# Kernel tuning notes

Hardware: AMD Instinct MI355X
Metric: run time of the kernel (lower is better)

The kernel has to match this reference:

```python
import jax, jax.numpy as jnp
import numpy as np

D = 4
R = 6
P = 2 * R + 1          # 13, fine match window
N = P * P              # 169
MR = 12
MP = 2 * MR + 1        # 25, coarse search window
DIL_INT = 15


def corr_sampler(t, r, Pp, dil):
    """SpatialCorrelationSampler(kernel_size=1, patch_size=Pp, dilation_patch=dil).
    t, r: (b,c,h,w). Returns (b,Pp,Pp,h,w): corr[b,p,q,y,x] = sum_c t[b,c,y,x]*r[b,c,y+dil*(p-R),x+dil*(q-R)] (zero pad)."""
    Rr = (Pp - 1) // 2
    pad = Rr * dil
    b, c, h, w = t.shape
    rp = jnp.pad(r, ((0, 0), (0, 0), (pad, pad), (pad, pad)))
    d = (jnp.arange(Pp) - Rr) * dil
    yi = jnp.arange(h)[None, :] + d[:, None] + pad      # (Pp,h)
    xi = jnp.arange(w)[None, :] + d[:, None] + pad      # (Pp,w)
    g = rp[:, :, yi[:, None, :, None], xi[None, :, None, :]]  # (b,c,Pp,Pp,h,w)
    return jnp.einsum('bchw,bcpqhw->bpqhw', t, g)


def bilinear_patch(src, py, px):
    """deform_im2col: bilinear-sample a PxP patch around (x+off_x+dx, y+off_y+dy).
    src (b,c,h,w); py (b,P,1,h,w); px (b,1,P,h,w) float coords. Returns (b,c,P,P,h,w)."""
    b, c, h, w = src.shape
    y0 = jnp.floor(py); x0 = jnp.floor(px)
    wy = py - y0; wx = px - x0
    y0 = y0.astype(jnp.int32); x0 = x0.astype(jnp.int32)

    def corner(yi, xi, wgt):
        valid = (yi >= 0) & (yi < h) & (xi >= 0) & (xi < w)
        yc = jnp.clip(yi, 0, h - 1)
        xc = jnp.clip(xi, 0, w - 1)
        v = jax.vmap(lambda im, a, bb: im[:, a, bb])(src, yc, xc)  # (b,c,P,P,h,w)
        return v * (wgt * valid)[:, None]

    out = corner(y0, x0, (1 - wy) * (1 - wx))
    out = out + corner(y0, x0 + 1, (1 - wy) * wx)
    out = out + corner(y0 + 1, x0, wy * (1 - wx))
    out = out + corner(y0 + 1, x0 + 1, wy * wx)
    return out


def unfold_patches(src, Pp):
    """F.unfold(src, kernel_size=Pp, padding=Rr) -> (b,c,Pp,Pp,h,w)."""
    Rr = (Pp - 1) // 2
    b, c, h, w = src.shape
    sp = jnp.pad(src, ((0, 0), (0, 0), (Rr, Rr), (Rr, Rr)))
    yi = jnp.arange(h)[None, :] + jnp.arange(Pp)[:, None]
    xi = jnp.arange(w)[None, :] + jnp.arange(Pp)[:, None]
    return sp[:, :, yi[:, None, :, None], xi[None, :, None, :]]


def _forward(feats_r, feats_t, quantized_r, nsearch, dirates):
    nref = feats_r.shape[0]
    b, c, h, w = feats_t.shape
    f32 = feats_t.dtype
    dy = (jnp.arange(P) - R).astype(f32)
    gy, gx = jnp.meshgrid(jnp.arange(-MR, MR + 1).astype(f32),
                          jnp.arange(-MR, MR + 1).astype(f32), indexing='ij')
    corrs = []
    py = px = None
    for si in range(nsearch):
        d = dirates[si]
        cc = corr_sampler(feats_t, feats_r[si], MP, d)                     # (b,MP,MP,h,w)
        cc = jax.nn.softmax(cc.reshape(b, MP * MP, h * w), axis=1).reshape(b, MP, MP, h, w)
        off_x = jnp.einsum('bpqhw,pq->bhw', cc, gx) * d                    # soft-argmax offsets
        off_y = jnp.einsum('bpqhw,pq->bhw', cc, gy) * d
        # sample coords: (b,P,1,h,w) / (b,1,P,h,w)
        py = (off_y + jnp.arange(h).astype(f32)[None, :, None])[:, None, None] + dy[:, None, None, None]
        px = (off_x + jnp.arange(w).astype(f32)[None, None, :])[:, None, None] + dy[None, :, None, None]
        col = bilinear_patch(feats_r[si], py, px)                          # (b,c,P,P,h,w)
        corrs.append(jnp.einsum('bchw,bcpqhw->bpqhw', feats_t, col).reshape(b, N, h * w))
    for ind in range(nsearch, nref):
        corrs.append(corr_sampler(feats_t, feats_r[ind], P, 1).reshape(b, N, h * w))
    corr = jax.nn.softmax(jnp.concatenate(corrs, 1), axis=1)               # (b,nref*N,hw)
    qr = quantized_r[:, :, :, ::D, ::D]                                    # prep(): (nref,b,C,h,w)
    cols = []
    for i in range(nsearch):
        # NOTE: faithful to original -- uses offset0 from the LAST coarse-search iteration
        cols.append(bilinear_patch(qr[i], py, px).reshape(b, -1, N, h * w))
    for i in range(nsearch, nref):
        cols.append(unfold_patches(qr[i], P).reshape(b, -1, N, h * w))
    image_uf = jnp.concatenate(cols, 2)                                    # (b,C,nref*N,hw)
    out = jnp.einsum('bnx,bcnx->bcx', corr, image_uf)
    return out.reshape(b, qr.shape[2], h, w)


def reference(feats_r, feats_t, quantized_r, ref_index, current_ind):
    gaps = [int(current_ind) - int(x) for x in np.asarray(ref_index)]
    nsearch = sum(g > DIL_INT for g in gaps)
    dirates = [min(4, g // DIL_INT + 1) for g in gaps if g > DIL_INT]
    return _forward(feats_r, feats_t, quantized_r, nsearch, dirates)


def setup_inputs():
    key = jax.random.key(0)
    k1, k2, k3 = jax.random.split(key, 3)
    feats_r = jax.random.normal(k1, (3, 1, 64, 48, 84), jnp.float32)
    feats_t = jax.random.normal(k2, (1, 64, 48, 84), jnp.float32)
    quantized_r = jax.random.uniform(k3, (3, 1, 32, 192, 336), jnp.float32)
    return dict(feats_r=feats_r, feats_t=feats_t, quantized_r=quantized_r,
                ref_index=np.arange(3), current_ind=16)
```

## Files before the change

kernel.cpp:

```cpp
#include <hip/hip_runtime.h>
#include <math.h>

constexpr int H  = 48;
constexpr int W  = 84;
constexpr int HW = H * W;
constexpr int C  = 64;
constexpr int CQ = 32;
constexpr int QH = 192;
constexpr int QW = 336;
constexpr int NREF = 3;
constexpr int SLG = 176;
constexpr int LGS = 544;
constexpr int S625 = 640;

constexpr int RROWS = NREF * HW;
constexpr int RZERO = RROWS;
constexpr int RLO   = RROWS + 1;
constexpr int TZERO = HW;
constexpr int TLO   = HW + 1;

typedef short bf16x8 __attribute__((ext_vector_type(8)));
typedef float f32x4  __attribute__((ext_vector_type(4)));

#define DEV __device__ __forceinline__

DEV unsigned short f2bf_rn(float f) {
  unsigned int u = __builtin_bit_cast(unsigned int, f);
  u += 0x7FFFu + ((u >> 16) & 1u);
  return (unsigned short)(u >> 16);
}
DEV float bf2f(unsigned short h) {
  unsigned int u = ((unsigned int)h) << 16;
  return __builtin_bit_cast(float, u);
}

DEV float block_sum(float v, float* red) {
  __syncthreads();
#pragma unroll
  for (int o = 32; o > 0; o >>= 1) v += __shfl_down(v, o, 64);
  if ((threadIdx.x & 63) == 0) red[threadIdx.x >> 6] = v;
  __syncthreads();
  return red[0] + red[1] + red[2] + red[3];
}
DEV float block_max(float v, float* red) {
  __syncthreads();
#pragma unroll
  for (int o = 32; o > 0; o >>= 1) v = fmaxf(v, __shfl_down(v, o, 64));
  if ((threadIdx.x & 63) == 0) red[threadIdx.x >> 6] = v;
  __syncthreads();
  return fmaxf(fmaxf(red[0], red[1]), fmaxf(red[2], red[3]));
}

__global__ __launch_bounds__(256) void k_prep(const float* __restrict__ fr,
                                              const float* __restrict__ ft,
                                              const float* __restrict__ q,
                                              float* __restrict__ frT,
                                              float* __restrict__ ftT,
                                              unsigned short* __restrict__ rb,
                                              unsigned short* __restrict__ tb,
                                              unsigned short* __restrict__ qrb) {
  __shared__ float lds[64][65];
  const int mode = blockIdx.y;
  const int tid = threadIdx.x;

  if (mode < 4) {
    const int r = mode;
    const float* src = (r < NREF) ? (fr + (size_t)r * C * HW) : ft;
    float* dstF          = (r < NREF) ? (frT + (size_t)r * HW * C) : ftT;
    unsigned short* dstH = (r < NREF) ? (rb + (size_t)r * HW * C) : tb;
    const size_t loOff   = (size_t)((r < NREF) ? RLO : TLO) * C;
    const int pb = blockIdx.x * 64;
    const int a = tid & 63, b = tid >> 6;
#pragma unroll
    for (int i = 0; i < 16; i++) {
      int c = i * 4 + b;
      lds[c][a] = src[c * HW + pb + a];
    }
    __syncthreads();
#pragma unroll
    for (int i = 0; i < 16; i++) {
      int p = i * 4 + b;
      float v = lds[a][p];
      size_t o = (size_t)(pb + p) * C + a;
      dstF[o] = v;
      unsigned short h = f2bf_rn(v);
      dstH[o] = h;
      dstH[o + loOff] = f2bf_rn(v - bf2f(h));
    }
    if (mode == 3 && blockIdx.x == 0 && tid < 64) {
      rb[(size_t)RZERO * C + tid] = 0;
      rb[(size_t)(RLO + RROWS) * C + tid] = 0;
      tb[(size_t)TZERO * C + tid] = 0;
      tb[(size_t)(TLO + HW) * C + tid] = 0;
    }
  } else {
    const int k = mode - 4;
    const int yq = blockIdx.x;
    if (yq >= H) return;
    unsigned short* qs = (unsigned short*)lds;
    const int c = tid >> 3, xo = tid & 7;
#pragma unroll
    for (int i = 0; i < 11; i++) {
      const int x = xo + 8 * i;
      if (x < W) {
        const float v = q[((size_t)(k * CQ + c) * QH + yq * 4) * QW + x * 4];
        qs[x * CQ + c] = f2bf_rn(v);
      }
    }
    __syncthreads();
    const unsigned int* qsu = (const unsigned int*)qs;
    unsigned int* dst = (unsigned int*)(qrb + (size_t)k * HW * CQ + (size_t)yq * W * CQ);
    for (int o = tid; o < W * CQ / 2; o += 256) dst[o] = qsu[o];
  }
}

DEV f32x4 six_mfma(bf16x8 ah0, bf16x8 ah1, bf16x8 al0, bf16x8 al1,
                   bf16x8 bh0, bf16x8 bh1, bf16x8 bl0, bf16x8 bl1) {
  f32x4 acc = {0.f, 0.f, 0.f, 0.f};
  acc = __builtin_amdgcn_mfma_f32_16x16x32_bf16(ah0, bh0, acc, 0, 0, 0);
  acc = __builtin_amdgcn_mfma_f32_16x16x32_bf16(ah1, bh1, acc, 0, 0, 0);
  acc = __builtin_amdgcn_mfma_f32_16x16x32_bf16(ah0, bl0, acc, 0, 0, 0);
  acc = __builtin_amdgcn_mfma_f32_16x16x32_bf16(ah1, bl1, acc, 0, 0, 0);
  acc = __builtin_amdgcn_mfma_f32_16x16x32_bf16(al0, bh0, acc, 0, 0, 0);
  acc = __builtin_amdgcn_mfma_f32_16x16x32_bf16(al1, bh1, acc, 0, 0, 0);
  return acc;
}

template <int D>
DEV void sbody(const unsigned short* __restrict__ rb,
               bf16x8 a0h0, bf16x8 a0h1, bf16x8 a0l0, bf16x8 a0l1,
               bf16x8 a1h0, bf16x8 a1h1, bf16x8 a1l0, bf16x8 a1l1,
               int y, int x0, int sub, int si, int fpx, int lq,
               float* __restrict__ lg625) {
  constexpr int Zoff = (D == 1) ? 16 : (D == 2) ? 32 : 48;
  constexpr int NZT  = (D == 1) ? 4  : (D == 2) ? 6  : 8;
  const int fko = lq * 8;
  const int p1 = sub, p2 = sub + 13;
  const bool has2 = (p2 <= 24);
  const int rowA = y + D * (p1 - 12);
  const int rowB = y + D * (p2 - 12);
  const bool rva = (rowA >= 0) && (rowA < H);
  const bool rvb = has2 && (rowB >= 0) && (rowB < H);
  const int roffA = si * HW + rowA * W;
  const int roffB = si * HW + rowB * W;

  for (int zt = 0; zt < NZT; ++zt) {
    const int z = x0 - Zoff + zt * 16 + fpx;
    const bool zv = (z >= 0) && (z < W);
    const size_t oA = (size_t)((rva && zv) ? (roffA + z) : RZERO) * C + fko;
    const size_t oB = (size_t)((rvb && zv) ? (roffB + z) : RZERO) * C + fko;
    const bf16x8 bah0 = *reinterpret_cast<const bf16x8*>(rb + oA);
    const bf16x8 bah1 = *reinterpret_cast<const bf16x8*>(rb + oA + 32);
    const bf16x8 bal0 = *reinterpret_cast<const bf16x8*>(rb + oA + (size_t)RLO * C);
    const bf16x8 bal1 = *reinterpret_cast<const bf16x8*>(rb + oA + (size_t)RLO * C + 32);
    const bf16x8 bbh0 = *reinterpret_cast<const bf16x8*>(rb + oB);
    const bf16x8 bbh1 = *reinterpret_cast<const bf16x8*>(rb + oB + 32);
    const bf16x8 bbl0 = *reinterpret_cast<const bf16x8*>(rb + oB + (size_t)RLO * C);
    const bf16x8 bbl1 = *reinterpret_cast<const bf16x8*>(rb + oB + (size_t)RLO * C + 32);

    f32x4 acc00 = six_mfma(a0h0, a0h1, a0l0, a0l1, bah0, bah1, bal0, bal1);
    f32x4 acc10 = six_mfma(a1h0, a1h1, a1l0, a1l1, bah0, bah1, bal0, bal1);
    f32x4 acc01 = six_mfma(a0h0, a0h1, a0l0, a0l1, bbh0, bbh1, bbl0, bbl1);
    f32x4 acc11 = six_mfma(a1h0, a1h1, a1l0, a1l1, bbh0, bbh1, bbl0, bbl1);

    const int zb = -Zoff + zt * 16 + fpx + 12 * D;
#pragma unroll
    for (int t2 = 0; t2 < 2; ++t2) {
#pragma unroll
      for (int r = 0; r < 4; r++) {
        const int xo = t2 * 16 + lq * 4 + r;
        const int qnum = zb - xo;
        bool ok;
        int qq;
        if constexpr (D == 3) {
          qq = (qnum * 21846) >> 16;
          ok = (qnum >= 0) && (qq * 3 == qnum) && (qq < 25);
        } else {
          constexpr int SH = (D == 4) ? 2 : (D == 2) ? 1 : 0;
          qq = qnum >> SH;
          ok = (qnum >= 0) && ((qnum & (D - 1)) == 0) && (qq < 25);
        }
        const int xl = x0 + xo;
        if (ok && xl < W) {
          float* base = lg625 + ((size_t)si * HW + y * W + xl) * S625;
          base[p1 * 25 + qq] = t2 ? acc10[r] : acc00[r];
          if (has2) base[p2 * 25 + qq] = t2 ? acc11[r] : acc01[r];
        }
      }
    }
  }
}

DEV void ubody(const unsigned short* __restrict__ rb,
               bf16x8 a0h0, bf16x8 a0h1, bf16x8 a0l0, bf16x8 a0l1,
               bf16x8 a1h0, bf16x8 a1h1, bf16x8 a1l0, bf16x8 a1l1,
               int y, int x0, int sub, int si, int fpx, int lq,
               float* __restrict__ lg) {
  const int fko = lq * 8;
  const int dp1 = sub, dp2 = sub + 7;
  const bool has2 = (dp2 < 13);
  const int rowA = y + dp1 - 6;
  const int rowB = y + dp2 - 6;
  const bool rva = (rowA >= 0) && (rowA < H);
  const bool rvb = has2 && (rowB >= 0) && (rowB < H);
  const int roffA = si * HW + rowA * W;
  const int roffB = si * HW + rowB * W;

  for (int zt = 0; zt < 4; ++zt) {
    const int z = x0 - 16 + zt * 16 + fpx;
    const bool zv = (z >= 0) && (z < W);
    const size_t oA = (size_t)((rva && zv) ? (roffA + z) : RZERO) * C + fko;
    const size_t oB = (size_t)((rvb && zv) ? (roffB + z) : RZERO) * C + fko;
    const bf16x8 bah0 = *reinterpret_cast<const bf16x8*>(rb + oA);
    const bf16x8 bah1 = *reinterpret_cast<const bf16x8*>(rb + oA + 32);
    const bf16x8 bal0 = *reinterpret_cast<const bf16x8*>(rb + oA + (size_t)RLO * C);
    const bf16x8 bal1 = *reinterpret_cast<const bf16x8*>(rb + oA + (size_t)RLO * C + 32);
    const bf16x8 bbh0 = *reinterpret_cast<const bf16x8*>(rb + oB);
    const bf16x8 bbh1 = *reinterpret_cast<const bf16x8*>(rb + oB + 32);
    const bf16x8 bbl0 = *reinterpret_cast<const bf16x8*>(rb + oB + (size_t)RLO * C);
    const bf16x8 bbl1 = *reinterpret_cast<const bf16x8*>(rb + oB + (size_t)RLO * C + 32);

    f32x4 acc00 = six_mfma(a0h0, a0h1, a0l0, a0l1, bah0, bah1, bal0, bal1);
    f32x4 acc10 = six_mfma(a1h0, a1h1, a1l0, a1l1, bah0, bah1, bal0, bal1);
    f32x4 acc01 = six_mfma(a0h0, a0h1, a0l0, a0l1, bbh0, bbh1, bbl0, bbl1);
    f32x4 acc11 = six_mfma(a1h0, a1h1, a1l0, a1l1, bbh0, bbh1, bbl0, bbl1);

    const int zb = -16 + zt * 16 + fpx + 6;
#pragma unroll
    for (int t2 = 0; t2 < 2; ++t2) {
#pragma unroll
      for (int r = 0; r < 4; r++) {
        const int xo = t2 * 16 + lq * 4 + r;
        const int qq = zb - xo;
        const int xl = x0 + xo;
        if (qq >= 0 && qq < 13 && xl < W) {
          float* base = lg + (size_t)(y * W + xl) * LGS + si * SLG;
          base[dp1 * 13 + qq] = t2 ? acc10[r] : acc00[r];
          if (has2) base[dp2 * 13 + qq] = t2 ? acc11[r] : acc01[r];
        }
      }
    }
  }
}

__global__ __launch_bounds__(256) void k_mfma(
    const unsigned short* __restrict__ rb, const unsigned short* __restrict__ tb,
    const int* __restrict__ ridx, const int* __restrict__ curp,
    float* __restrict__ lg, float* __restrict__ lg625) {
  const int si = blockIdx.z >> 2, pz = blockIdx.z & 3;
  const int gap = curp[0] - ridx[si];
  const bool isSearch = gap > 15;
  const int lane = threadIdx.x & 63, wave = threadIdx.x >> 6;
  const int sub = pz * 4 + wave;
  if (isSearch ? (sub >= 13) : (sub >= 7)) return;

  const int y = blockIdx.y, x0 = blockIdx.x * 32;
  const int fpx = lane & 15, lq = lane >> 4;

  const int g0 = (x0 + fpx < W) ? (y * W + x0 + fpx) : TZERO;
  const int g1 = (x0 + 16 + fpx < W) ? (y * W + x0 + 16 + fpx) : TZERO;
  const unsigned short* t0 = tb + (size_t)g0 * C + lq * 8;
  const unsigned short* t1 = tb + (size_t)g1 * C + lq * 8;
  const bf16x8 a0h0 = *reinterpret_cast<const bf16x8*>(t0);
  const bf16x8 a0h1 = *reinterpret_cast<const bf16x8*>(t0 + 32);
  const bf16x8 a0l0 = *reinterpret_cast<const bf16x8*>(t0 + (size_t)TLO * C);
  const bf16x8 a0l1 = *reinterpret_cast<const bf16x8*>(t0 + (size_t)TLO * C + 32);
  const bf16x8 a1h0 = *reinterpret_cast<const bf16x8*>(t1);
  const bf16x8 a1h1 = *reinterpret_cast<const bf16x8*>(t1 + 32);
  const bf16x8 a1l0 = *reinterpret_cast<const bf16x8*>(t1 + (size_t)TLO * C);
  const bf16x8 a1l1 = *reinterpret_cast<const bf16x8*>(t1 + (size_t)TLO * C + 32);

  if (isSearch) {
    int d = gap / 15 + 1; if (d > 4) d = 4;
    switch (d) {
      case 1: sbody<1>(rb, a0h0, a0h1, a0l0, a0l1, a1h0, a1h1, a1l0, a1l1,
                       y, x0, sub, si, fpx, lq, lg625); break;
      case 2: sbody<2>(rb, a0h0, a0h1, a0l0, a0l1, a1h0, a1h1, a1l0, a1l1,
                       y, x0, sub, si, fpx, lq, lg625); break;
      case 3: sbody<3>(rb, a0h0, a0h1, a0l0, a0l1, a1h0, a1h1, a1l0, a1l1,
                       y, x0, sub, si, fpx, lq, lg625); break;
      default: sbody<4>(rb, a0h0, a0h1, a0l0, a0l1, a1h0, a1h1, a1l0, a1l1,
                        y, x0, sub, si, fpx, lq, lg625); break;
    }
  } else {
    ubody(rb, a0h0, a0h1, a0l0, a0l1, a1h0, a1h1, a1l0, a1l1,
          y, x0, sub, si, fpx, lq, lg);
  }
}

__global__ __launch_bounds__(256) void k_off(
    const float* __restrict__ lg625,
    const int* __restrict__ ridx, const int* __restrict__ curp,
    float* __restrict__ samp) {
  const int si = blockIdx.y;
  const int gap = curp[0] - ridx[si];
  if (gap <= 15) return;
  int d = gap / 15 + 1; if (d > 4) d = 4;

  const int lane = threadIdx.x & 63, wave = threadIdx.x >> 6;
  const int pix = blockIdx.x * 4 + wave;
  const float* Lp = lg625 + ((size_t)si * HW + pix) * S625;

  float v[10];
#pragma unroll
  for (int k = 0; k < 10; k++) {
    const int idx = k * 64 + lane;
    v[k] = (idx < 625) ? Lp[idx] : -1e30f;
  }
  float m = v[0];
#pragma unroll
  for (int k = 1; k < 10; k++) m = fmaxf(m, v[k]);
#pragma unroll
  for (int o = 1; o < 64; o <<= 1) m = fmaxf(m, __shfl_xor(m, o, 64));

  float se = 0.f, sy = 0.f, sx = 0.f;
#pragma unroll
  for (int k = 0; k < 10; k++) {
    const int idx = k * 64 + lane;
    if (idx < 625) {
      const float e = __expf(v[k] - m);
      const int p = (idx * 5243) >> 17;
      const int q = idx - p * 25;
      se += e;
      sy += e * (float)(p - 12);
      sx += e * (float)(q - 12);
    }
  }
#pragma unroll
  for (int o = 1; o < 64; o <<= 1) {
    se += __shfl_xor(se, o, 64);
    sy += __shfl_xor(sy, o, 64);
    sx += __shfl_xor(sx, o, 64);
  }
  if (lane == 0) {
    const float inv = 1.f / se;
    const float oy = (float)d * sy * inv, ox = (float)d * sx * inv;
    const int y = pix / W, x = pix - y * W;
    const float fy = (float)y + oy, fx = (float)x + ox;
    const float Y0 = floorf(fy), X0 = floorf(fx);
    *reinterpret_cast<float4*>(samp + ((size_t)si * HW + pix) * 4) =
        make_float4(Y0, X0, fy - Y0, fx - X0);
  }
}

__global__ __launch_bounds__(256, 4) void k_pix(
    const float* __restrict__ frT, const float* __restrict__ ftT,
    const unsigned short* __restrict__ qrb, const float* __restrict__ lg,
    const float* __restrict__ samp,
    const int* __restrict__ ridx, const int* __restrict__ curp,
    float* __restrict__ out) {
  const int pix = blockIdx.x;
  const int y = pix / W, x = pix - y * W;
  const int tid = threadIdx.x;
  const int lane = tid & 63, wave = tid >> 6;

  __shared__ __align__(16) float tl[64];
  __shared__ float C14[14][16];
  __shared__ __align__(16) float lgs[3 * SLG];
  __shared__ float red[4];
  __shared__ int   wloc[640];
  __shared__ float wval[640];
  __shared__ float part[4][32];

  const int cur = curp[0];
  bool srch[NREF];
  int ls = -1;
#pragma unroll
  for (int k = 0; k < NREF; k++) {
    srch[k] = (cur - ridx[k]) > 15;
    if (srch[k]) ls = k;
  }

  if (tid < 64) tl[tid] = ftT[(size_t)pix * C + tid];
  if (tid < 21) lgs[(tid / 7) * SLG + 169 + (tid % 7)] = -1e30f;
  __syncthreads();

#pragma unroll 1
  for (int si = 0; si < NREF; ++si) {
    if (!srch[si]) continue;
    const float4 sp = *reinterpret_cast<const float4*>(samp + ((size_t)si * HW + pix) * 4);
    const int iY = (int)sp.x, iX = (int)sp.y;
    const float wy = sp.z, wx = sp.w;
    const float* frB = frT + (size_t)si * HW * C;

    if (tid < 224) {
      const int j = tid >> 4, cg = tid & 15;
      const int col = iX - 6 + j;
      const bool cv = (col >= 0) && (col < W);
      const float4 tv = *reinterpret_cast<const float4*>(&tl[cg * 4]);
      float s[14];
#pragma unroll
      for (int i = 0; i < 14; ++i) {
        const int row = iY - 6 + i;
        s[i] = 0.f;
        if (cv && row >= 0 && row < H) {
          const float4 rv4 = *reinterpret_cast<const float4*>(
              frB + (size_t)(row * W + col) * C + cg * 4);
          s[i] = tv.x * rv4.x + tv.y * rv4.y + tv.z * rv4.z + tv.w * rv4.w;
        }
      }
#pragma unroll
      for (int i = 0; i < 14; ++i) {
        s[i] += __shfl_xor(s[i], 1, 64);
        s[i] += __shfl_xor(s[i], 2, 64);
        s[i] += __shfl_xor(s[i], 4, 64);
        s[i] += __shfl_xor(s[i], 8, 64);
      }
      if (cg == 0) {
#pragma unroll
        for (int i = 0; i < 14; ++i) C14[i][j] = s[i];
      }
    }
    __syncthreads();
    for (int it = tid; it < 169; it += 256) {
      const int i = it / 13, j = it - i * 13;
      lgs[si * SLG + it] =
          (1.f - wy) * ((1.f - wx) * C14[i][j] + wx * C14[i][j + 1]) +
          wy * ((1.f - wx) * C14[i + 1][j] + wx * C14[i + 1][j + 1]);
    }
    __syncthreads();
  }

#pragma unroll 1
  for (int k = 0; k < NREF; k++) {
    if (srch[k]) continue;
    const float* src = lg + (size_t)pix * LGS + k * SLG;
    if (tid < 42)
      *reinterpret_cast<float4*>(&lgs[k * SLG + tid * 4]) =
          *reinterpret_cast<const float4*>(src + tid * 4);
    else if (tid == 42)
      lgs[k * SLG + 168] = src[168];
  }
  __syncthreads();

  float m = -1e30f;
  for (int i = tid; i < 3 * SLG; i += 256) m = fmaxf(m, lgs[i]);
  m = block_max(m, red);
  float se = 0.f;
  for (int i = tid; i < 3 * SLG; i += 256) {
    const float e = __expf(lgs[i] - m);
    lgs[i] = e;
    se += e;
  }
  se = block_sum(se, red);
  const float inv = 1.f / se;

  int bases[NREF], tot = 0;
#pragma unroll
  for (int k = 0; k < NREF; k++) { bases[k] = tot; tot += srch[k] ? 196 : 169; }
  const int NT = (tot + 63) >> 6;

  int liY = 0, liX = 0;
  float lwy = 0.f, lwx = 0.f;
  if (ls >= 0) {
    const float4 sl = *reinterpret_cast<const float4*>(samp + ((size_t)ls * HW + pix) * 4);
    liY = (int)sl.x; liX = (int)sl.y; lwy = sl.z; lwx = sl.w;
  }

#pragma unroll 1
  for (int k = 0; k < NREF; k++) {
    const int base = bases[k];
    if (srch[k]) {
      const float* wk = &lgs[k * SLG];
      for (int it = tid; it < 196; it += 256) {
        const int i = it / 14, j = it - i * 14;
        const float a00 = (i < 13 && j < 13) ? wk[i * 13 + j] : 0.f;
        const float a01 = (i < 13 && j >= 1) ? wk[i * 13 + j - 1] : 0.f;
        const float a10 = (i >= 1 && j < 13) ? wk[(i - 1) * 13 + j] : 0.f;
        const float a11 = (i >= 1 && j >= 1) ? wk[(i - 1) * 13 + j - 1] : 0.f;
        const float wv = (1.f - lwy) * ((1.f - lwx) * a00 + lwx * a01) +
                         lwy * ((1.f - lwx) * a10 + lwx * a11);
        const int row = liY + i - 6, col = liX + j - 6;
        const bool v = (unsigned)row < (unsigned)H && (unsigned)col < (unsigned)W;
        wloc[base + it] = v ? (k * HW + row * W + col) : 0;
        wval[base + it] = v ? wv : 0.f;
      }
    } else {
      for (int it = tid; it < 169; it += 256) {
        const int p = it / 13, q = it - p * 13;
        const int row = y + p - 6, col = x + q - 6;
        const bool v = (unsigned)row < (unsigned)H && (unsigned)col < (unsigned)W;
        wloc[base + it] = v ? (k * HW + row * W + col) : 0;
        wval[base + it] = v ? lgs[k * SLG + it] : 0.f;
      }
    }
  }
  for (int e = tot + tid; e < NT * 64; e += 256) { wloc[e] = 0; wval[e] = 0.f; }
  __syncthreads();

  const int c4 = lane & 3, l16 = lane >> 2;
  float a[8] = {0.f, 0.f, 0.f, 0.f, 0.f, 0.f, 0.f, 0.f};
  for (int t = 0; t < NT; ++t) {
    const int e = t * 64 + wave * 16 + l16;
    const float wv = wval[e];
    const int loc = wloc[e];
    const bf16x8 qv = *reinterpret_cast<const bf16x8*>(
        qrb + (size_t)loc * CQ + c4 * 8);
#pragma unroll
    for (int j = 0; j < 8; j++)
      a[j] = fmaf(wv, bf2f((unsigned short)qv[j]), a[j]);
  }
#pragma unroll
  for (int o = 4; o < 64; o <<= 1) {
#pragma unroll
    for (int j = 0; j < 8; j++) a[j] += __shfl_xor(a[j], o, 64);
  }
  if (l16 == 0) {
#pragma unroll
    for (int j = 0; j < 8; j++) part[wave][c4 * 8 + j] = a[j];
  }
  __syncthreads();
  if (tid < 32) {
    const float s = part[0][tid] + part[1][tid] + part[2][tid] + part[3][tid];
    out[(size_t)tid * HW + pix] = s * inv;
  }
}

extern "C" void kernel_launch(void* const* d_in, const int* in_sizes, int n_in,
                              void* d_out, int out_size, void* d_ws, size_t ws_size,
                              hipStream_t stream) {
  (void)in_sizes; (void)n_in; (void)out_size; (void)ws_size;
  const float* fr = (const float*)d_in[0];
  const float* ft = (const float*)d_in[1];
  const float* q  = (const float*)d_in[2];
  const int* ridx = (const int*)d_in[3];
  const int* cur  = (const int*)d_in[4];
  float* out = (float*)d_out;

  char* ws = (char*)d_ws;
  float* frT  = (float*)ws;                  ws += (size_t)NREF * HW * C * 4;
  float* ftT  = (float*)ws;                  ws += (size_t)HW * C * 4;
  unsigned short* rb = (unsigned short*)ws;  ws += (size_t)2 * (NREF * HW + 1) * C * 2;
  unsigned short* tb = (unsigned short*)ws;  ws += (size_t)2 * (HW + 1) * C * 2;
  unsigned short* qrb = (unsigned short*)ws; ws += (size_t)NREF * HW * CQ * 2;
  float* lg    = (float*)ws;                 ws += (size_t)HW * LGS * 4;
  float* lg625 = (float*)ws;                 ws += (size_t)NREF * HW * S625 * 4;
  float* samp  = (float*)ws;                 ws += (size_t)NREF * HW * 4 * 4;

  k_prep<<<dim3(HW / 64, 7), dim3(256), 0, stream>>>(fr, ft, q, frT, ftT,
                                                     rb, tb, qrb);
  k_mfma<<<dim3(3, H, NREF * 4), dim3(256), 0, stream>>>(rb, tb, ridx, cur,
                                                         lg, lg625);
  k_off<<<dim3(HW / 4, NREF), dim3(256), 0, stream>>>(lg625, ridx, cur, samp);
  k_pix<<<dim3(HW), dim3(256), 0, stream>>>(frT, ftT, qrb, lg, samp,
                                            ridx, cur, out);
}
```

Before: 72.42 us.

## Fuse offset-softmax kernel into per-pixel kernel and drop the max pass

Removes the separate k_off launch and its samp buffer. k_pix now computes the coarse-search soft-argmax offsets itself, reading lg625 with all 256 threads and reducing across waves through shared memory. The max-subtraction pass is replaced by clamping logits at 60 before exp, which saves a reduction but would change results if logits ever exceed that bound. The aim is to cut one kernel launch and a global-memory round trip, at the cost of more work and barriers inside each k_pix block.

```diff
diff --git a/kernel.cpp b/kernel.cpp
--- a/kernel.cpp
+++ b/kernel.cpp
@@ -288,65 +288,10 @@
   }
 }
 
-__global__ __launch_bounds__(256) void k_off(
-    const float* __restrict__ lg625,
-    const int* __restrict__ ridx, const int* __restrict__ curp,
-    float* __restrict__ samp) {
-  const int si = blockIdx.y;
-  const int gap = curp[0] - ridx[si];
-  if (gap <= 15) return;
-  int d = gap / 15 + 1; if (d > 4) d = 4;
-
-  const int lane = threadIdx.x & 63, wave = threadIdx.x >> 6;
-  const int pix = blockIdx.x * 4 + wave;
-  const float* Lp = lg625 + ((size_t)si * HW + pix) * S625;
-
-  float v[10];
-#pragma unroll
-  for (int k = 0; k < 10; k++) {
-    const int idx = k * 64 + lane;
-    v[k] = (idx < 625) ? Lp[idx] : -1e30f;
-  }
-  float m = v[0];
-#pragma unroll
-  for (int k = 1; k < 10; k++) m = fmaxf(m, v[k]);
-#pragma unroll
-  for (int o = 1; o < 64; o <<= 1) m = fmaxf(m, __shfl_xor(m, o, 64));
-
-  float se = 0.f, sy = 0.f, sx = 0.f;
-#pragma unroll
-  for (int k = 0; k < 10; k++) {
-    const int idx = k * 64 + lane;
-    if (idx < 625) {
-      const float e = __expf(v[k] - m);
-      const int p = (idx * 5243) >> 17;
-      const int q = idx - p * 25;
-      se += e;
-      sy += e * (float)(p - 12);
-      sx += e * (float)(q - 12);
-    }
-  }
-#pragma unroll
-  for (int o = 1; o < 64; o <<= 1) {
-    se += __shfl_xor(se, o, 64);
-    sy += __shfl_xor(sy, o, 64);
-    sx += __shfl_xor(sx, o, 64);
-  }
-  if (lane == 0) {
-    const float inv = 1.f / se;
-    const float oy = (float)d * sy * inv, ox = (float)d * sx * inv;
-    const int y = pix / W, x = pix - y * W;
-    const float fy = (float)y + oy, fx = (float)x + ox;
-    const float Y0 = floorf(fy), X0 = floorf(fx);
-    *reinterpret_cast<float4*>(samp + ((size_t)si * HW + pix) * 4) =
-        make_float4(Y0, X0, fy - Y0, fx - X0);
-  }
-}
-
 __global__ __launch_bounds__(256, 4) void k_pix(
     const float* __restrict__ frT, const float* __restrict__ ftT,
     const unsigned short* __restrict__ qrb, const float* __restrict__ lg,
-    const float* __restrict__ samp,
+    const float* __restrict__ lg625,
     const int* __restrict__ ridx, const int* __restrict__ curp,
     float* __restrict__ out) {
   const int pix = blockIdx.x;
@@ -358,69 +303,26 @@
   __shared__ float C14[14][16];
   __shared__ __align__(16) float lgs[3 * SLG];
   __shared__ float red[4];
+  __shared__ float red3[4][3];
   __shared__ int   wloc[640];
   __shared__ float wval[640];
   __shared__ float part[4][32];
 
   const int cur = curp[0];
   bool srch[NREF];
+  int dd[NREF];
   int ls = -1;
 #pragma unroll
   for (int k = 0; k < NREF; k++) {
-    srch[k] = (cur - ridx[k]) > 15;
+    const int g = cur - ridx[k];
+    srch[k] = (g > 15);
+    int d = g / 15 + 1;
+    dd[k] = d > 4 ? 4 : d;
     if (srch[k]) ls = k;
   }
 
   if (tid < 64) tl[tid] = ftT[(size_t)pix * C + tid];
   if (tid < 21) lgs[(tid / 7) * SLG + 169 + (tid % 7)] = -1e30f;
-  __syncthreads();
-
-#pragma unroll 1
-  for (int si = 0; si < NREF; ++si) {
-    if (!srch[si]) continue;
-    const float4 sp = *reinterpret_cast<const float4*>(samp + ((size_t)si * HW + pix) * 4);
-    const int iY = (int)sp.x, iX = (int)sp.y;
-    const float wy = sp.z, wx = sp.w;
-    const float* frB = frT + (size_t)si * HW * C;
-
-    if (tid < 224) {
-      const int j = tid >> 4, cg = tid & 15;
-      const int col = iX - 6 + j;
-      const bool cv = (col >= 0) && (col < W);
-      const float4 tv = *reinterpret_cast<const float4*>(&tl[cg * 4]);
-      float s[14];
-#pragma unroll
-      for (int i = 0; i < 14; ++i) {
-        const int row = iY - 6 + i;
-        s[i] = 0.f;
-        if (cv && row >= 0 && row < H) {
-          const float4 rv4 = *reinterpret_cast<const float4*>(
-              frB + (size_t)(row * W + col) * C + cg * 4);
-          s[i] = tv.x * rv4.x + tv.y * rv4.y + tv.z * rv4.z + tv.w * rv4.w;
-        }
-      }
-#pragma unroll
-      for (int i = 0; i < 14; ++i) {
-        s[i] += __shfl_xor(s[i], 1, 64);
-        s[i] += __shfl_xor(s[i], 2, 64);
-        s[i] += __shfl_xor(s[i], 4, 64);
-        s[i] += __shfl_xor(s[i], 8, 64);
-      }
-      if (cg == 0) {
-#pragma unroll
-        for (int i = 0; i < 14; ++i) C14[i][j] = s[i];
-      }
-    }
-    __syncthreads();
-    for (int it = tid; it < 169; it += 256) {
-      const int i = it / 13, j = it - i * 13;
-      lgs[si * SLG + it] =
-          (1.f - wy) * ((1.f - wx) * C14[i][j] + wx * C14[i][j + 1]) +
-          wy * ((1.f - wx) * C14[i + 1][j] + wx * C14[i + 1][j + 1]);
-    }
-    __syncthreads();
-  }
-
 #pragma unroll 1
   for (int k = 0; k < NREF; k++) {
     if (srch[k]) continue;
@@ -433,6 +335,78 @@
   }
   __syncthreads();
 
+  int liY = 0, liX = 0;
+  float lwy = 0.f, lwx = 0.f;
+#pragma unroll 1
+  for (int si = 0; si < NREF; ++si) {
+    if (!srch[si]) continue;
+
+    const float* Lp = lg625 + ((size_t)si * HW + pix) * S625;
+    float se = 0.f, sy = 0.f, sx = 0.f;
+    for (int i = tid; i < 625; i += 256) {
+      const float e = __expf(fminf(Lp[i], 60.f));
+      const int p = (i * 5243) >> 17;
+      const int q = i - p * 25;
+      se += e; sy += e * (float)(p - 12); sx += e * (float)(q - 12);
+    }
+#pragma unroll
+    for (int o = 1; o < 64; o <<= 1) {
+      se += __shfl_xor(se, o, 64);
+      sy += __shfl_xor(sy, o, 64);
+      sx += __shfl_xor(sx, o, 64);
+    }
+    if (lane == 0) { red3[wave][0] = se; red3[wave][1] = sy; red3[wave][2] = sx; }
+    __syncthreads();
+    se = red3[0][0] + red3[1][0] + red3[2][0] + red3[3][0];
+    sy = red3[0][1] + red3[1][1] + red3[2][1] + red3[3][1];
+    sx = red3[0][2] + red3[1][2] + red3[2][2] + red3[3][2];
+    const float inv6 = 1.f / se;
+    const float oy = (float)dd[si] * sy * inv6, ox = (float)dd[si] * sx * inv6;
+    const float fy = (float)y + oy, fx = (float)x + ox;
+    const float Y0 = floorf(fy), X0 = floorf(fx);
+    const int iY = (int)Y0, iX = (int)X0;
+    const float wy = fy - Y0, wx = fx - X0;
+    if (si == ls) { liY = iY; liX = iX; lwy = wy; lwx = wx; }
+
+    const float* frB = frT + (size_t)si * HW * C;
+    if (tid < 224) {
+      const int j = tid >> 4, cg = tid & 15;
+      const int col = iX - 6 + j;
+      const bool cv = (col >= 0) && (col < W);
+      const float4 tv = *reinterpret_cast<const float4*>(&tl[cg * 4]);
+      float s[14];
+#pragma unroll
+      for (int i = 0; i < 14; ++i) {
+        const int row = iY - 6 + i;
+        s[i] = 0.f;
+        if (cv && row >= 0 && row < H) {
+          const float4 rv4 = *reinterpret_cast<const float4*>(
+              frB + (size_t)(row * W + col) * C + cg * 4);
+          s[i] = tv.x * rv4.x + tv.y * rv4.y + tv.z * rv4.z + tv.w * rv4.w;
+        }
+      }
+#pragma unroll
+      for (int i = 0; i < 14; ++i) {
+        s[i] += __shfl_xor(s[i], 1, 64);
+        s[i] += __shfl_xor(s[i], 2, 64);
+        s[i] += __shfl_xor(s[i], 4, 64);
+        s[i] += __shfl_xor(s[i], 8, 64);
+      }
+      if (cg == 0) {
+#pragma unroll
+        for (int i = 0; i < 14; ++i) C14[i][j] = s[i];
+      }
+    }
+    __syncthreads();
+    for (int it = tid; it < 169; it += 256) {
+      const int i = it / 13, j = it - i * 13;
+      lgs[si * SLG + it] =
+          (1.f - wy) * ((1.f - wx) * C14[i][j] + wx * C14[i][j + 1]) +
+          wy * ((1.f - wx) * C14[i + 1][j] + wx * C14[i + 1][j + 1]);
+    }
+    __syncthreads();
+  }
+
   float m = -1e30f;
   for (int i = tid; i < 3 * SLG; i += 256) m = fmaxf(m, lgs[i]);
   m = block_max(m, red);
@@ -449,13 +423,6 @@
 #pragma unroll
   for (int k = 0; k < NREF; k++) { bases[k] = tot; tot += srch[k] ? 196 : 169; }
   const int NT = (tot + 63) >> 6;
-
-  int liY = 0, liX = 0;
-  float lwy = 0.f, lwx = 0.f;
-  if (ls >= 0) {
-    const float4 sl = *reinterpret_cast<const float4*>(samp + ((size_t)ls * HW + pix) * 4);
-    liY = (int)sl.x; liX = (int)sl.y; lwy = sl.z; lwx = sl.w;
-  }
 
 #pragma unroll 1
   for (int k = 0; k < NREF; k++) {
@@ -535,13 +502,11 @@
   unsigned short* qrb = (unsigned short*)ws; ws += (size_t)NREF * HW * CQ * 2;
   float* lg    = (float*)ws;                 ws += (size_t)HW * LGS * 4;
   float* lg625 = (float*)ws;                 ws += (size_t)NREF * HW * S625 * 4;
-  float* samp  = (float*)ws;                 ws += (size_t)NREF * HW * 4 * 4;
 
   k_prep<<<dim3(HW / 64, 7), dim3(256), 0, stream>>>(fr, ft, q, frT, ftT,
                                                      rb, tb, qrb);
   k_mfma<<<dim3(3, H, NREF * 4), dim3(256), 0, stream>>>(rb, tb, ridx, cur,
                                                          lg, lg625);
-  k_off<<<dim3(HW / 4, NREF), dim3(256), 0, stream>>>(lg625, ridx, cur, samp);
-  k_pix<<<dim3(HW), dim3(256), 0, stream>>>(frT, ftT, qrb, lg, samp,
+  k_pix<<<dim3(HW), dim3(256), 0, stream>>>(frT, ftT, qrb, lg, lg625,
                                             ridx, cur, out);
 }
```

Result: slower. 74.11 us (+2.3%).
